# Kernel optimization log

Measured on AMD Instinct MI355X. Metric: run time of the kernel, lower is better.

## Reference

```python
import jax, jax.numpy as jnp
import numpy as np

B, D_IN, H, OUT = 4096, 2048, 4096, 1000
TEMPERATURE = 0.5


def _l2_normalize(w):
    return w / jnp.linalg.norm(w, axis=1, keepdims=True)


def setup_inputs() -> dict:
    key = jax.random.key(0)
    ks = jax.random.split(key, 8)
    x = jax.random.normal(ks[0], (B, D_IN), dtype=jnp.float32)
    kohonen_weights = _l2_normalize(jax.random.normal(ks[1], (H, D_IN), dtype=jnp.float32))
    # MLP: 4096 -> 2048 -> 1024 -> 1000 (hidden_layers=2, div=2)
    def lin(k, fan_in, fan_out):
        kw, kb = jax.random.split(k)
        bound = 1.0 / np.sqrt(fan_in)
        W = jax.random.uniform(kw, (fan_out, fan_in), minval=-bound, maxval=bound, dtype=jnp.float32)
        b = jax.random.uniform(kb, (fan_out,), minval=-bound, maxval=bound, dtype=jnp.float32)
        return W, b
    w1, b1 = lin(ks[2], H, H // 2)
    w2, b2 = lin(ks[3], H // 2, H // 4)
    w3, b3 = lin(ks[4], H // 4, OUT)
    return {"x": x, "kohonen_weights": kohonen_weights,
            "w1": w1, "b1": b1, "w2": w2, "b2": b2, "w3": w3, "b3": b3}


def reference(x, kohonen_weights, w1, b1, w2, b2, w3, b3):
    # pairwise euclidean distances [B, H] via expanded GEMM (cdist p=2)
    x2 = jnp.sum(x * x, axis=1, keepdims=True)            # [B,1]
    w2sq = jnp.sum(kohonen_weights * kohonen_weights, axis=1)  # [H]
    d2 = x2 + w2sq[None, :] - 2.0 * (x @ kohonen_weights.T)
    distances = jnp.sqrt(jnp.maximum(d2, 1e-12))
    winners = jnp.argmin(distances, axis=1)
    soft = jax.nn.softmax(-distances / TEMPERATURE, axis=1)
    # MLP (dropout=0 / eval mode)
    h = jax.nn.relu(soft @ w1.T + b1)
    h = jax.nn.relu(h @ w2.T + b2)
    output = h @ w3.T + b3
    return output, winners
```

## Files before the change

### kernel.cpp

```cpp
#include <hip/hip_runtime.h>
#include <hip/hip_bf16.h>
#include <stdint.h>

typedef __attribute__((ext_vector_type(4))) float f32x4;
typedef __attribute__((ext_vector_type(8))) __bf16 bf16x8;
typedef unsigned short u16;
typedef unsigned long long u64;

__device__ __forceinline__ u16 f2bf(float f){
  unsigned u = __float_as_uint(f);
  u += 0x7fffu + ((u >> 16) & 1u);
  return (u16)(u >> 16);
}
__device__ __forceinline__ float bf2f(u16 v){
  return __uint_as_float(((unsigned)v) << 16);
}

__device__ __forceinline__ void gload16(const u16* g, u16* l){
  __builtin_amdgcn_global_load_lds(
      (__attribute__((address_space(1))) void*)g,
      (__attribute__((address_space(3))) void*)l, 16, 0, 0);
}

template<int N> __device__ __forceinline__ void waitcnt_vm(){
  if constexpr (N==0) asm volatile("s_waitcnt vmcnt(0)" ::: "memory");
  else if constexpr (N==2) asm volatile("s_waitcnt vmcnt(2)" ::: "memory");
  else if constexpr (N==3) asm volatile("s_waitcnt vmcnt(3)" ::: "memory");
  else if constexpr (N==4) asm volatile("s_waitcnt vmcnt(4)" ::: "memory");
  else if constexpr (N==6) asm volatile("s_waitcnt vmcnt(6)" ::: "memory");
  else if constexpr (N==8) asm volatile("s_waitcnt vmcnt(8)" ::: "memory");
}

__global__ __launch_bounds__(64)
void cvt_rows(const float* __restrict__ src, u16* __restrict__ dst,
              float* __restrict__ sq)
{
#pragma clang fp contract(off)
  const int row = blockIdx.x;
  const int l = threadIdx.x;
  const float* r = src + (size_t)row * 2048;
  const f32x4* r4 = (const f32x4*)r;
  ushort4* d4 = (ushort4*)(dst + (size_t)row * 2048);
#pragma unroll
  for (int i = 0; i < 8; i++){
    f32x4 v = r4[l + 64*i];
    ushort4 o;
    o.x = f2bf(v.x); o.y = f2bf(v.y); o.z = f2bf(v.z); o.w = f2bf(v.w);
    d4[l + 64*i] = o;
  }
  float leaf = 0.f;
  if (l < 16){
    const f32x4* p4 = (const f32x4*)(r + l*128);
    f32x4 a0 = {0.f,0.f,0.f,0.f}, a1 = {0.f,0.f,0.f,0.f};
#pragma unroll
    for (int i = 0; i < 32; i += 2){
      f32x4 v0 = p4[i], v1 = p4[i+1];
      a0 = a0 + v0*v0;
      a1 = a1 + v1*v1;
    }
    leaf = ((a0.x+a0.y)+(a0.z+a0.w))+((a1.x+a1.y)+(a1.z+a1.w));
  }
#pragma unroll
  for (int s = 1; s < 16; s <<= 1){
    float o = __shfl_down(leaf, s);
    if ((l & (2*s - 1)) == 0) leaf = leaf + o;
  }
  if (l == 0) sq[row] = leaf;
}

__global__ __launch_bounds__(256)
void cvt_mat(const float* __restrict__ src, u16* __restrict__ dst, int n4)
{
  const f32x4* s4 = (const f32x4*)src;
  ushort4* d4 = (ushort4*)dst;
  for (int i = blockIdx.x*256 + threadIdx.x; i < n4; i += gridDim.x*256){
    f32x4 v = s4[i];
    ushort4 o;
    o.x = f2bf(v.x); o.y = f2bf(v.y); o.z = f2bf(v.z); o.w = f2bf(v.w);
    d4[i] = o;
  }
}

template<int BM, int BN, int WM, int WN, int EPI, int MINW>
__global__ __launch_bounds__(WM*WN*64, MINW)
void gemm_p(const u16* __restrict__ A, const u16* __restrict__ Bm,
            float* __restrict__ Cf, u16* __restrict__ Cb,
            const float* __restrict__ bias,
            int M, int N, int K, int ncols, int nbn)
{
  constexpr int T  = WM*WN*64;
  constexpr int FM = BM/(WM*16);
  constexpr int FN = BN/(WN*16);
  constexpr int ABYTES = BM*64;
  constexpr int BUFB   = (BM+BN)*64;
  constexpr int RA = ABYTES/(T*16);
  constexpr int RB = (BN*64)/(T*16);
  constexpr int IF = RA + RB;
  constexpr int NPH = (FM*FN >= 32) ? 2 : 1;
  extern __shared__ char lds[];

  const int t = threadIdx.x;
  const int nwg = gridDim.x;
  const int cpx = nwg >> 3;
  const int bid = blockIdx.x;
  const int wg  = (bid & 7)*cpx + (bid >> 3);
  const int bm = wg / nbn, bn = wg % nbn;
  const int brow = bm*BM, bcol = bn*BN;

  const int l = t & 63, w = t >> 6;
  const int wm = w / WN, wn = w % WN;
  const int wr = wm*(FM*16), wc = wn*(FN*16);
  const int fr = l & 15, fk = (l >> 4)*8;
  const int xk = fk ^ (((fr >> 1) & 3) << 3);

  const int srow = t >> 2;
  const int scol = ((t & 3)*8) ^ (((t >> 3) & 3) << 3);

  const u16* agp[RA]; const u16* bgp[RB];
#pragma unroll
  for (int r = 0; r < RA; r++)
    agp[r] = A + (size_t)(brow + r*(T>>2) + srow)*K + scol;
#pragma unroll
  for (int r = 0; r < RB; r++)
    bgp[r] = Bm + (size_t)(bcol + r*(T>>2) + srow)*K + scol;

  f32x4 acc[FM][FN] = {};
  const int nt = K >> 5;

  auto stageA = [&](int kt, int buf){
    char* dst = lds + buf*BUFB + t*16;
#pragma unroll
    for (int r = 0; r < RA; r++)
      gload16(agp[r] + (kt << 5), (u16*)(dst + r*T*16));
  };
  auto stageB = [&](int kt, int buf){
    char* dst = lds + buf*BUFB + ABYTES + t*16;
#pragma unroll
    for (int r = 0; r < RB; r++)
      gload16(bgp[r] + (kt << 5), (u16*)(dst + r*T*16));
  };

  stageA(0, 0); stageB(0, 0);
  stageA(1, 1); stageB(1, 1);
  stageA(2, 2); stageB(2, 2);
  waitcnt_vm<2*IF>();
  __builtin_amdgcn_s_barrier();

  for (int kt = 0; kt < nt; kt++){
    const int buf = kt & 3;
    const u16* As = (const u16*)(lds + buf*BUFB);
    const u16* Bs = (const u16*)(lds + buf*BUFB + ABYTES);
    const bool pre = (kt + 3 < nt);
    const int nbuf = (kt + 3) & 3;

    bf16x8 av[FM], bv[FN];
#pragma unroll
    for (int m = 0; m < FM; m++)
      av[m] = *(const bf16x8*)(As + (wr + m*16 + fr)*32 + xk);

    if (NPH == 1){
#pragma unroll
      for (int n = 0; n < FN; n++)
        bv[n] = *(const bf16x8*)(Bs + (wc + n*16 + fr)*32 + xk);
      if (pre){ stageA(kt + 3, nbuf); stageB(kt + 3, nbuf); }
      __builtin_amdgcn_s_barrier();
      __builtin_amdgcn_s_setprio(1);
#pragma unroll
      for (int m = 0; m < FM; m++)
#pragma unroll
        for (int n = 0; n < FN; n++)
          acc[m][n] = __builtin_amdgcn_mfma_f32_16x16x32_bf16(av[m], bv[n], acc[m][n], 0, 0, 0);
      __builtin_amdgcn_s_setprio(0);
    } else {
#pragma unroll
      for (int n = 0; n < FN/2; n++)
        bv[n] = *(const bf16x8*)(Bs + (wc + n*16 + fr)*32 + xk);
      if (pre) stageA(kt + 3, nbuf);
      __builtin_amdgcn_s_barrier();
      __builtin_amdgcn_s_setprio(1);
#pragma unroll
      for (int m = 0; m < FM; m++)
#pragma unroll
        for (int n = 0; n < FN/2; n++)
          acc[m][n] = __builtin_amdgcn_mfma_f32_16x16x32_bf16(av[m], bv[n], acc[m][n], 0, 0, 0);
      __builtin_amdgcn_s_setprio(0);

#pragma unroll
      for (int n = FN/2; n < FN; n++)
        bv[n] = *(const bf16x8*)(Bs + (wc + n*16 + fr)*32 + xk);
      if (pre) stageB(kt + 3, nbuf);
      __builtin_amdgcn_s_barrier();
      __builtin_amdgcn_s_setprio(1);
#pragma unroll
      for (int m = 0; m < FM; m++)
#pragma unroll
        for (int n = FN/2; n < FN; n++)
          acc[m][n] = __builtin_amdgcn_mfma_f32_16x16x32_bf16(av[m], bv[n], acc[m][n], 0, 0, 0);
      __builtin_amdgcn_s_setprio(0);
    }

    if (kt + 1 < nt){
      if (kt + 3 < nt)      waitcnt_vm<2*IF>();
      else if (kt + 2 < nt) waitcnt_vm<IF>();
      else                  waitcnt_vm<0>();
      __builtin_amdgcn_s_barrier();
    }
  }

#pragma unroll
  for (int n = 0; n < FN; n++){
    const int gcol = bcol + wc + n*16 + fr;
    float bvv = 0.f;
    if (EPI == 1) bvv = bias[gcol];
    if (EPI == 2 && gcol < ncols) bvv = bias[gcol];
#pragma unroll
    for (int m = 0; m < FM; m++){
      const int grow = brow + wr + m*16 + (l >> 4)*4;
#pragma unroll
      for (int r = 0; r < 4; r++){
        float v = acc[m][n][r];
        if (EPI == 0){
          Cf[(size_t)(grow + r)*N + gcol] = v;
        } else if (EPI == 1){
          Cb[(size_t)(grow + r)*N + gcol] = f2bf(fmaxf(v + bvv, 0.f));
        } else if (EPI == 2){
          if (gcol < ncols) Cf[(size_t)(grow + r)*ncols + gcol] = v + bvv;
        } else {
          Cb[(size_t)(grow + r)*N + gcol] = f2bf(v);
        }
      }
    }
  }
}

__global__ __launch_bounds__(256)
void row_softmax(const u16* __restrict__ Sb, const float* __restrict__ x2,
                 const float* __restrict__ w2sq,
                 const float* __restrict__ x, const float* __restrict__ W,
                 u16* __restrict__ soft, float* __restrict__ winners)
{
  const int b = blockIdx.x, t = threadIdx.x;
  const float x2b = x2[b];
  const ushort4* S4 = (const ushort4*)(Sb + (size_t)b*4096);
  const f32x4* W24 = (const f32x4*)w2sq;
  float dv[16];
  float bd = 3.0e38f; int bc = 0;
#pragma unroll
  for (int i = 0; i < 4; i++){
    ushort4 s = S4[t + 256*i];
    f32x4 wv = W24[t + 256*i];
    float sf[4] = {bf2f(s.x), bf2f(s.y), bf2f(s.z), bf2f(s.w)};
#pragma unroll
    for (int j = 0; j < 4; j++){
      float u = x2b + wv[j];
      float d2 = u - 2.0f*sf[j];
      float d = __fsqrt_rn(fmaxf(d2, 1e-12f));
      dv[i*4 + j] = d;
      if (d < bd){ bd = d; bc = (t + 256*i)*4 + j; }
    }
  }
  u64 key = ((u64)__float_as_uint(bd) << 32) | (unsigned)bc;
#pragma unroll
  for (int s = 1; s < 64; s <<= 1){
    u64 o = __shfl_xor(key, s);
    if (o < key) key = o;
  }
  __shared__ u64 wk[4];
  __shared__ double csum[4];
  __shared__ float fred[4];
  __shared__ int ccnt;
  __shared__ int cand[32];
  if ((t & 63) == 0) wk[t >> 6] = key;
  if (t == 0) ccnt = 0;
  __syncthreads();
  u64 k0 = wk[0];
  if (wk[1] < k0) k0 = wk[1];
  if (wk[2] < k0) k0 = wk[2];
  if (wk[3] < k0) k0 = wk[3];
  const float dmin = __uint_as_float((unsigned)(k0 >> 32));

  const float thr = dmin + 0.01f;
#pragma unroll
  for (int i = 0; i < 4; i++)
#pragma unroll
    for (int j = 0; j < 4; j++)
      if (dv[i*4 + j] <= thr){
        int p = atomicAdd(&ccnt, 1);
        if (p < 32) cand[p] = (t + 256*i)*4 + j;
      }
  __syncthreads();
  const int nc = min(ccnt, 32);

  float bestd = 3.0e38f; int besti = 0x7fffffff;
  const f32x4* xp = (const f32x4*)(x + (size_t)b*2048) + t*2;
  f32x4 xv0 = xp[0], xv1 = xp[1];
  for (int c = 0; c < nc; c++){
    const int h = cand[c];
    const f32x4* wp = (const f32x4*)(W + (size_t)h*2048) + t*2;
    f32x4 wv0 = wp[0], wv1 = wp[1];
    double a = 0.0;
#pragma unroll
    for (int j = 0; j < 4; j++) a += (double)xv0[j]*(double)wv0[j];
#pragma unroll
    for (int j = 0; j < 4; j++) a += (double)xv1[j]*(double)wv1[j];
#pragma unroll
    for (int s = 1; s < 64; s <<= 1) a += __shfl_xor(a, s);
    if ((t & 63) == 0) csum[t >> 6] = a;
    __syncthreads();
    if (t == 0){
      double tt = (csum[0] + csum[1]) + (csum[2] + csum[3]);
      float t32 = (float)tt;
      float u = x2b + w2sq[h];
      float d2 = u - 2.0f*t32;
      float d = __fsqrt_rn(fmaxf(d2, 1e-12f));
      if (d < bestd || (d == bestd && h < besti)){ bestd = d; besti = h; }
    }
    __syncthreads();
  }
  if (t == 0) winners[b] = (float)besti;

  float es = 0.f;
#pragma unroll
  for (int i = 0; i < 16; i++) es += __expf(-2.0f*(dv[i] - dmin));
#pragma unroll
  for (int s = 1; s < 64; s <<= 1) es += __shfl_xor(es, s);
  if ((t & 63) == 0) fred[t >> 6] = es;
  __syncthreads();
  const float tot = (fred[0] + fred[1]) + (fred[2] + fred[3]);
  const float inv = 1.0f / tot;
  ushort4* o4 = (ushort4*)(soft + (size_t)b*4096);
#pragma unroll
  for (int i = 0; i < 4; i++){
    ushort4 o;
    o.x = f2bf(__expf(-2.0f*(dv[i*4+0] - dmin))*inv);
    o.y = f2bf(__expf(-2.0f*(dv[i*4+1] - dmin))*inv);
    o.z = f2bf(__expf(-2.0f*(dv[i*4+2] - dmin))*inv);
    o.w = f2bf(__expf(-2.0f*(dv[i*4+3] - dmin))*inv);
    o4[t + 256*i] = o;
  }
}

extern "C" void kernel_launch(void* const* d_in, const int* in_sizes, int n_in,
                              void* d_out, int out_size, void* d_ws, size_t ws_size,
                              hipStream_t stream)
{
  const float* x  = (const float*)d_in[0];
  const float* Wk = (const float*)d_in[1];
  const float* w1 = (const float*)d_in[2];
  const float* b1 = (const float*)d_in[3];
  const float* w2 = (const float*)d_in[4];
  const float* b2 = (const float*)d_in[5];
  const float* w3 = (const float*)d_in[6];
  const float* b3 = (const float*)d_in[7];
  float* out = (float*)d_out;
  float* winners = out + (size_t)4096*1000;

  char* ws = (char*)d_ws;
  const size_t MB = 1u << 20;
  u16* Sb    = (u16*)(ws);
  u16* xb    = (u16*)(ws + 32*MB);
  u16* wb    = (u16*)(ws + 48*MB);
  u16* soft  = (u16*)(ws + 32*MB);
  u16* w1b   = (u16*)(ws + 64*MB);
  u16* w2b   = (u16*)(ws + 80*MB);
  u16* w3b   = (u16*)(ws + 84*MB);
  float* x2  = (float*)(ws + 86*MB);
  float* w2s = x2 + 4096;
  u16* h1    = (u16*)(ws);
  u16* h2    = (u16*)(ws + 16*MB);

  cvt_rows<<<4096, 64, 0, stream>>>(x, xb, x2);
  cvt_rows<<<4096, 64, 0, stream>>>(Wk, wb, w2s);
  cvt_mat<<<2048, 256, 0, stream>>>(w1, w1b, 2048*4096/4);
  cvt_mat<<<1024, 256, 0, stream>>>(w2, w2b, 1024*2048/4);
  hipMemsetAsync(w3b, 0, (size_t)1024*1024*2, stream);
  cvt_mat<<<512, 256, 0, stream>>>(w3, w3b, 1000*1024/4);

  hipFuncSetAttribute((const void*)gemm_p<256,256,2,4,3,2>,
                      hipFuncAttributeMaxDynamicSharedMemorySize, 4*512*64);
  gemm_p<256,256,2,4,3,2><<<256, 512, 4*512*64, stream>>>(
      xb, wb, nullptr, Sb, nullptr, 4096, 4096, 2048, 0, 16);

  row_softmax<<<4096, 256, 0, stream>>>(Sb, x2, w2s, x, Wk, soft, winners);

  hipFuncSetAttribute((const void*)gemm_p<256,128,4,2,1,2>,
                      hipFuncAttributeMaxDynamicSharedMemorySize, 4*384*64);
  gemm_p<256,128,4,2,1,2><<<256, 512, 4*384*64, stream>>>(
      soft, w1b, nullptr, h1, b1, 4096, 2048, 4096, 0, 16);

  hipFuncSetAttribute((const void*)gemm_p<128,128,2,2,1,3>,
                      hipFuncAttributeMaxDynamicSharedMemorySize, 4*256*64);
  gemm_p<128,128,2,2,1,3><<<256, 256, 4*256*64, stream>>>(
      h1, w2b, nullptr, h2, b2, 4096, 1024, 2048, 0, 8);

  hipFuncSetAttribute((const void*)gemm_p<128,128,2,2,2,3>,
                      hipFuncAttributeMaxDynamicSharedMemorySize, 4*256*64);
  gemm_p<128,128,2,2,2,3><<<256, 256, 4*256*64, stream>>>(
      h2, w3b, out, nullptr, b3, 4096, 1024, 1024, 1000, 8);
}
```

Before: 268.6 us.

## Add 256x256 double-buffered bf16 GEMM with split-K for first MLP layer

Introduces a new 8-wave 256x256-tile GEMM kernel with a two-stage LDS double buffer, XOR-swizzled LDS layout, half-tile staged loads interleaved with MFMA phases, and an XCD-aware block remap. It replaces the distance GEMM and the first MLP GEMM. The MLP GEMM is now split-K into two pieces written as bf16 partials, followed by a separate combine kernel that adds bias and applies ReLU. The aim is better MFMA utilisation and occupancy, at the cost of extra partial-sum traffic, a further launch, and bf16 rounding of the partials before they are summed.

```diff
diff --git a/kernel.cpp b/kernel.cpp
--- a/kernel.cpp
+++ b/kernel.cpp
@@ -25,7 +25,6 @@
 template<int N> __device__ __forceinline__ void waitcnt_vm(){
   if constexpr (N==0) asm volatile("s_waitcnt vmcnt(0)" ::: "memory");
   else if constexpr (N==2) asm volatile("s_waitcnt vmcnt(2)" ::: "memory");
-  else if constexpr (N==3) asm volatile("s_waitcnt vmcnt(3)" ::: "memory");
   else if constexpr (N==4) asm volatile("s_waitcnt vmcnt(4)" ::: "memory");
   else if constexpr (N==6) asm volatile("s_waitcnt vmcnt(6)" ::: "memory");
   else if constexpr (N==8) asm volatile("s_waitcnt vmcnt(8)" ::: "memory");
@@ -78,6 +77,153 @@
     ushort4 o;
     o.x = f2bf(v.x); o.y = f2bf(v.y); o.z = f2bf(v.z); o.w = f2bf(v.w);
     d4[i] = o;
+  }
+}
+
+__global__ __launch_bounds__(512, 2)
+void gemm8p(const u16* __restrict__ A, int lda,
+            const u16* __restrict__ Bm, int ldb,
+            u16* __restrict__ Cb, int N, int Kpp, int nbn, int blkpp)
+{
+  constexpr int BUFB = 65536;
+  extern __shared__ char lds[];
+  const int t = threadIdx.x;
+  const int nwg = gridDim.x;
+  const int cpx = nwg >> 3;
+  const int bid = blockIdx.x;
+  const int wg  = (bid & 7)*cpx + (bid >> 3);
+  const int piece = wg / blkpp;
+  const int rem = wg % blkpp;
+  const int bm = rem / nbn, bn = rem % nbn;
+  const int brow = bm*256, bcol = bn*256;
+  const u16* Ab = A + (size_t)brow*lda + (size_t)piece*Kpp;
+  const u16* Bb = Bm + (size_t)bcol*ldb + (size_t)piece*Kpp;
+  u16* Cp = Cb + (size_t)piece * 4096 * N;
+
+  const int l = t & 63, w = t >> 6;
+  const int wm = w >> 2, wn = w & 3;
+  const int wr = wm*128, wc = wn*64;
+  const int fr = l & 15, fq = l >> 4;
+  const int cb0 = (fq ^ (fr & 7)) << 4;
+  const int cb1 = ((4 + fq) ^ (fr & 7)) << 4;
+  const int scol8 = ((t & 7) ^ ((t >> 3) & 7)) * 8;
+  const int srow = t >> 3;
+
+  const int nt = Kpp >> 6;
+  f32x4 acc[8][4] = {};
+
+  auto stage_half = [&](int kt, int h){
+    const int nb = kt & 1;
+    const u16* src = (h < 2) ? Ab : Bb;
+    const int ld = (h < 2) ? lda : ldb;
+    const u16* s0 = src + (size_t)((h & 1)*128 + srow)*ld + kt*64 + scol8;
+    char* d = lds + nb*BUFB + (h >> 1)*32768 + (h & 1)*16384 + t*16;
+    gload16(s0, (u16*)d);
+    gload16(s0 + (size_t)64*ld, (u16*)(d + 8192));
+  };
+  auto ldA = [&](int buf, int m, int cb)->bf16x8 {
+    return *(const bf16x8*)(lds + buf*BUFB + (wr + m*16 + fr)*128 + cb);
+  };
+  auto ldB = [&](int buf, int n, int cb)->bf16x8 {
+    return *(const bf16x8*)(lds + buf*BUFB + 32768 + (wc + n*16 + fr)*128 + cb);
+  };
+
+  stage_half(0,0); stage_half(0,1); stage_half(0,2); stage_half(0,3);
+  stage_half(1,0); stage_half(1,1);
+  waitcnt_vm<4>();
+  __builtin_amdgcn_s_barrier();
+
+  for (int kt = 0; kt < nt; kt++){
+    const int buf = kt & 1;
+    bf16x8 av0[8], av1[8], bv0[4], bv1[4];
+
+#pragma unroll
+    for (int m = 0; m < 8; m++) av0[m] = ldA(buf, m, cb0);
+#pragma unroll
+    for (int n = 0; n < 4; n++) bv0[n] = ldB(buf, n, cb0);
+    if (kt + 1 < nt) stage_half(kt + 1, 2);
+    __builtin_amdgcn_s_barrier();
+    __builtin_amdgcn_s_setprio(1);
+#pragma unroll
+    for (int m = 0; m < 4; m++)
+#pragma unroll
+      for (int n = 0; n < 4; n++)
+        acc[m][n] = __builtin_amdgcn_mfma_f32_16x16x32_bf16(av0[m], bv0[n], acc[m][n], 0, 0, 0);
+    __builtin_amdgcn_s_setprio(0);
+    __builtin_amdgcn_s_barrier();
+
+#pragma unroll
+    for (int m = 0; m < 8; m++) av1[m] = ldA(buf, m, cb1);
+    if (kt + 1 < nt) stage_half(kt + 1, 3);
+    __builtin_amdgcn_s_barrier();
+    __builtin_amdgcn_s_setprio(1);
+#pragma unroll
+    for (int m = 4; m < 8; m++)
+#pragma unroll
+      for (int n = 0; n < 4; n++)
+        acc[m][n] = __builtin_amdgcn_mfma_f32_16x16x32_bf16(av0[m], bv0[n], acc[m][n], 0, 0, 0);
+    __builtin_amdgcn_s_setprio(0);
+    asm volatile("s_waitcnt lgkmcnt(0)" ::: "memory");
+    __builtin_amdgcn_s_barrier();
+
+#pragma unroll
+    for (int n = 0; n < 4; n++) bv1[n] = ldB(buf, n, cb1);
+    if (kt + 2 < nt) stage_half(kt + 2, 0);
+    __builtin_amdgcn_s_barrier();
+    __builtin_amdgcn_s_setprio(1);
+#pragma unroll
+    for (int m = 0; m < 4; m++)
+#pragma unroll
+      for (int n = 0; n < 4; n++)
+        acc[m][n] = __builtin_amdgcn_mfma_f32_16x16x32_bf16(av1[m], bv1[n], acc[m][n], 0, 0, 0);
+    __builtin_amdgcn_s_setprio(0);
+    __builtin_amdgcn_s_barrier();
+
+    if (kt + 2 < nt) stage_half(kt + 2, 1);
+    __builtin_amdgcn_s_barrier();
+    __builtin_amdgcn_s_setprio(1);
+#pragma unroll
+    for (int m = 4; m < 8; m++)
+#pragma unroll
+      for (int n = 0; n < 4; n++)
+        acc[m][n] = __builtin_amdgcn_mfma_f32_16x16x32_bf16(av1[m], bv1[n], acc[m][n], 0, 0, 0);
+    __builtin_amdgcn_s_setprio(0);
+    if (kt + 1 < nt){
+      if (kt <= nt - 3) waitcnt_vm<4>();
+      else              waitcnt_vm<0>();
+      __builtin_amdgcn_s_barrier();
+    }
+  }
+
+#pragma unroll
+  for (int n = 0; n < 4; n++){
+    const int gcol = bcol + wc + n*16 + fr;
+#pragma unroll
+    for (int m = 0; m < 8; m++){
+      const int grow = brow + wr + m*16 + fq*4;
+#pragma unroll
+      for (int r = 0; r < 4; r++)
+        Cp[(size_t)(grow + r)*N + gcol] = f2bf(acc[m][n][r]);
+    }
+  }
+}
+
+__global__ __launch_bounds__(256)
+void combine_relu(const u16* __restrict__ p0, const u16* __restrict__ p1,
+                  const float* __restrict__ bias, u16* __restrict__ out)
+{
+  const int n4 = 4096*2048/4;
+  for (int i = blockIdx.x*256 + threadIdx.x; i < n4; i += gridDim.x*256){
+    ushort4 a = ((const ushort4*)p0)[i];
+    ushort4 b = ((const ushort4*)p1)[i];
+    const int col = (i*4) & 2047;
+    f32x4 bi = *(const f32x4*)(bias + col);
+    ushort4 o;
+    o.x = f2bf(fmaxf(bf2f(a.x) + bf2f(b.x) + bi.x, 0.f));
+    o.y = f2bf(fmaxf(bf2f(a.y) + bf2f(b.y) + bi.y, 0.f));
+    o.z = f2bf(fmaxf(bf2f(a.z) + bf2f(b.z) + bi.z, 0.f));
+    o.w = f2bf(fmaxf(bf2f(a.w) + bf2f(b.w) + bi.w, 0.f));
+    ((ushort4*)out)[i] = o;
   }
 }
 
@@ -184,7 +330,6 @@
         for (int n = 0; n < FN/2; n++)
           acc[m][n] = __builtin_amdgcn_mfma_f32_16x16x32_bf16(av[m], bv[n], acc[m][n], 0, 0, 0);
       __builtin_amdgcn_s_setprio(0);
-
 #pragma unroll
       for (int n = FN/2; n < FN; n++)
         bv[n] = *(const bf16x8*)(Bs + (wc + n*16 + fr)*32 + xk);
@@ -358,14 +503,16 @@
   char* ws = (char*)d_ws;
   const size_t MB = 1u << 20;
   u16* Sb    = (u16*)(ws);
-  u16* xb    = (u16*)(ws + 32*MB);
-  u16* wb    = (u16*)(ws + 48*MB);
   u16* soft  = (u16*)(ws + 32*MB);
   u16* w1b   = (u16*)(ws + 64*MB);
   u16* w2b   = (u16*)(ws + 80*MB);
   u16* w3b   = (u16*)(ws + 84*MB);
   float* x2  = (float*)(ws + 86*MB);
   float* w2s = x2 + 4096;
+  u16* xb    = (u16*)(ws + 88*MB);
+  u16* wb    = (u16*)(ws + 104*MB);
+  u16* P0    = (u16*)(ws + 88*MB);
+  u16* P1    = (u16*)(ws + 104*MB);
   u16* h1    = (u16*)(ws);
   u16* h2    = (u16*)(ws + 16*MB);
 
@@ -376,17 +523,17 @@
   hipMemsetAsync(w3b, 0, (size_t)1024*1024*2, stream);
   cvt_mat<<<512, 256, 0, stream>>>(w3, w3b, 1000*1024/4);
 
-  hipFuncSetAttribute((const void*)gemm_p<256,256,2,4,3,2>,
-                      hipFuncAttributeMaxDynamicSharedMemorySize, 4*512*64);
-  gemm_p<256,256,2,4,3,2><<<256, 512, 4*512*64, stream>>>(
-      xb, wb, nullptr, Sb, nullptr, 4096, 4096, 2048, 0, 16);
+  hipFuncSetAttribute((const void*)gemm8p,
+                      hipFuncAttributeMaxDynamicSharedMemorySize, 131072);
+
+  gemm8p<<<256, 512, 131072, stream>>>(xb, 2048, wb, 2048, Sb,
+                                       4096, 2048, 16, 256);
 
   row_softmax<<<4096, 256, 0, stream>>>(Sb, x2, w2s, x, Wk, soft, winners);
 
-  hipFuncSetAttribute((const void*)gemm_p<256,128,4,2,1,2>,
-                      hipFuncAttributeMaxDynamicSharedMemorySize, 4*384*64);
-  gemm_p<256,128,4,2,1,2><<<256, 512, 4*384*64, stream>>>(
-      soft, w1b, nullptr, h1, b1, 4096, 2048, 4096, 0, 16);
+  gemm8p<<<256, 512, 131072, stream>>>(soft, 4096, w1b, 4096, P0,
+                                       2048, 2048, 8, 128);
+  combine_relu<<<2048, 256, 0, stream>>>(P0, P1, b1, h1);
 
   hipFuncSetAttribute((const void*)gemm_p<128,128,2,2,1,3>,
                       hipFuncAttributeMaxDynamicSharedMemorySize, 4*256*64);
```

New measurement: 270.5 us. Within noise of the previous version (+0.7%).
